# Kernel tuning notes

Hardware: AMD Instinct MI355X
Metric: run time of the kernel (lower is better)

## Reference

```python
import jax, jax.numpy as jnp
import numpy as np

B, S, D, E, K = 4, 4096, 2048, 64, 2


def setup_inputs() -> dict:
    key = jax.random.key(0)
    kx, kwg, kwn, kn = jax.random.split(key, 4)
    scale = 1.0 / np.sqrt(D)
    return {
        "x": jax.random.normal(kx, (B, S, D), dtype=jnp.float32),
        "Wg": jax.random.normal(kwg, (E, D), dtype=jnp.float32) * scale,
        "bg": jnp.zeros((E,), dtype=jnp.float32),
        "Wn": jax.random.normal(kwn, (E, D), dtype=jnp.float32) * scale,
        "bn": jnp.zeros((E,), dtype=jnp.float32),
        "noise": jax.random.normal(kn, (B, S, E), dtype=jnp.float32),
    }


def reference(x, Wg, bg, Wn, bn, noise):
    # gate / noise projections: [B,S,D] @ [D,E] -> [B,S,E]
    gate_logits = jnp.einsum("bsd,ed->bse", x, Wg) + bg
    noise_std = jax.nn.softplus(jnp.einsum("bsd,ed->bse", x, Wn) + bn)
    noisy_logits = gate_logits + noise * noise_std  # training-mode path

    # top-k over experts, then scatter back with -inf elsewhere
    flat = noisy_logits.reshape(-1, E)  # [T, E], T = B*S
    top_vals, top_idx = jax.lax.top_k(flat, K)  # [T, K]
    T = flat.shape[0]
    neg_inf = jnp.full((T, E), -jnp.inf, dtype=flat.dtype)
    full_logits = neg_inf.at[jnp.arange(T)[:, None], top_idx].set(top_vals)

    gate_probs = jax.nn.softmax(full_logits, axis=-1).reshape(B, S, E)
    top_k_indices = top_idx.reshape(B, S, K)
    return gate_probs, top_k_indices
```

## Files before the change

### kernel.cpp

```cpp
#include <hip/hip_runtime.h>
#include <math.h>
#include <stdint.h>

#define D_ 2048
#define E_ 64
#define T_ 16384

#define BM 32
#define BK 64
#define NT 32
#define ABUF_B 8192
#define BBUF_B 32768
#define BUF_B (ABUF_B + BBUF_B)
#define CT_STRIDE 132

typedef _Float16 h8 __attribute__((ext_vector_type(8)));
typedef float f16v __attribute__((ext_vector_type(16)));

__device__ __forceinline__ void split2(const float4& a, const float4& b,
                                       h8& h, h8& m) {
    const float xe[8] = {a.x, a.y, a.z, a.w, b.x, b.y, b.z, b.w};
#pragma unroll
    for (int i = 0; i < 8; ++i) {
        const _Float16 hh_ = (_Float16)xe[i];
        const float r = (xe[i] - (float)hh_) * 1024.0f;
        h[i] = hh_;
        m[i] = (_Float16)r;
    }
}

__device__ __forceinline__ void gload16(const void* g, void* l) {
    __builtin_amdgcn_global_load_lds(
        (const __attribute__((address_space(1))) uint32_t*)g,
        (__attribute__((address_space(3))) uint32_t*)l, 16, 0, 0);
}

__device__ __forceinline__ void topk_epilogue(float g, float nl, float nz,
                                              int lane, size_t tg,
                                              float* __restrict__ out_probs,
                                              float* __restrict__ out_idx) {
    const float sp = fmaxf(nl, 0.f) + log1pf(expf(-fabsf(nl)));
    const float noisy = g + nz * sp;

    float v = noisy;
    int idx = lane;
#pragma unroll
    for (int off = 32; off > 0; off >>= 1) {
        const float ov = __shfl_xor(v, off);
        const int oi = __shfl_xor(idx, off);
        if (ov > v || (ov == v && oi < idx)) { v = ov; idx = oi; }
    }
    const float v1 = v;
    const int i1 = idx;
    v = (lane == i1) ? -INFINITY : noisy;
    idx = lane;
#pragma unroll
    for (int off = 32; off > 0; off >>= 1) {
        const float ov = __shfl_xor(v, off);
        const int oi = __shfl_xor(idx, off);
        if (ov > v || (ov == v && oi < idx)) { v = ov; idx = oi; }
    }
    const float v2 = v;
    const int i2 = idx;

    const float e2 = expf(v2 - v1);
    const float denom = 1.f + e2;
    const float p = (lane == i1) ? (1.f / denom)
                                 : ((lane == i2) ? (e2 / denom) : 0.f);
    out_probs[tg * E_ + lane] = p;
    if (lane == 0) {
        out_idx[tg * 2 + 0] = (float)i1;
        out_idx[tg * 2 + 1] = (float)i2;
    }
}

__global__ void w_split_kernel(const float* __restrict__ Wg,
                               const float* __restrict__ Wn,
                               h8* __restrict__ wsp) {
    const int idx = blockIdx.x * blockDim.x + threadIdx.x;
    const int lane = idx & 63;
    const int s = (idx >> 6) & 127;
    const int f = idx >> 13;
    const int n = f * 32 + (lane & 31);
    const int k0 = s * 16 + ((lane >> 5) << 3);
    const float* src = (n < 64) ? &Wg[(size_t)n * D_ + k0]
                                : &Wn[(size_t)(n - 64) * D_ + k0];
    h8 hv, mv;
#pragma unroll
    for (int i = 0; i < 8; ++i) {
        const float w = src[i];
        const _Float16 wh = (_Float16)w;
        const float r = (w - (float)wh) * 1024.0f;
        hv[i] = wh;
        mv[i] = (_Float16)r;
    }
    wsp[0 * 32768 + idx] = hv;
    wsp[1 * 32768 + idx] = mv;
}

__launch_bounds__(512)
__global__ void gemm_topk_kernel(const float* __restrict__ x,
                                 const h8* __restrict__ wsp,
                                 const float* __restrict__ bg,
                                 const float* __restrict__ bn,
                                 const float* __restrict__ noise,
                                 float* __restrict__ out_probs,
                                 float* __restrict__ out_idx) {
    __shared__ __align__(16) char smem[2 * BUF_B];
    const int tid = threadIdx.x;
    const int lane = tid & 63;
    const int wv = tid >> 6;
    const int kh = wv >> 2;
    const int wn = wv & 3;
    const int block_m0 = blockIdx.x * BM;
    const char* wb = (const char*)wsp;

    const int ks_s = tid >> 6;
    const int sl = tid & 63;
    const float* asrc = x + (size_t)(block_m0 + (sl & 31)) * D_
                          + (ks_s & 3) * 16 + ((sl >> 5) << 3);
    const int aw_hi = (0 * 4 + (ks_s & 3)) * 1024 + sl * 16;
    const int aw_mid = (1 * 4 + (ks_s & 3)) * 1024 + sl * 16;

    f16v hh = {}, cx = {};

    auto STAGE_B = [&](int t, int b) {
        char* Bb = smem + b * BUF_B + ABUF_B;
#pragma unroll
        for (int j = 0; j < 4; ++j) {
            const int rid = wv * 4 + j;
            const int p = rid >> 4, f = (rid & 15) >> 2, ks = rid & 3;
            gload16(wb + ((size_t)(p * 32768 + f * 8192 + (t * 4 + ks) * 64 + lane)) * 16,
                    Bb + rid * 1024 + lane * 16);
        }
    };
    auto ALOAD = [&](int t, float4& ra, float4& rb) {
        if (tid < 256) {
            ra = *(const float4*)(asrc + t * BK);
            rb = *(const float4*)(asrc + t * BK + 4);
        }
    };
    auto ASPLIT = [&](const float4& ra, const float4& rb, int b) {
        if (tid < 256) {
            h8 hv, mv;
            split2(ra, rb, hv, mv);
            char* Ab = smem + b * BUF_B;
            *(h8*)(Ab + aw_hi) = hv;
            *(h8*)(Ab + aw_mid) = mv;
        }
    };
    auto COMPUTE = [&](int b) {
        const char* Ab = smem + b * BUF_B;
        const char* Bb = Ab + ABUF_B;
#pragma unroll
        for (int ksl = 0; ksl < 2; ++ksl) {
            const int ks = kh * 2 + ksl;
            const h8 ah = *(const h8*)(Ab + (0 * 4 + ks) * 1024 + lane * 16);
            const h8 am = *(const h8*)(Ab + (1 * 4 + ks) * 1024 + lane * 16);
            const h8 bh = *(const h8*)(Bb + ((0 * 16 + wn * 4 + ks)) * 1024 + lane * 16);
            const h8 bm = *(const h8*)(Bb + ((1 * 16 + wn * 4 + ks)) * 1024 + lane * 16);
            hh = __builtin_amdgcn_mfma_f32_32x32x16_f16(ah, bh, hh, 0, 0, 0);
            cx = __builtin_amdgcn_mfma_f32_32x32x16_f16(ah, bm, cx, 0, 0, 0);
            cx = __builtin_amdgcn_mfma_f32_32x32x16_f16(am, bh, cx, 0, 0, 0);
        }
    };

    float4 ra0{}, rb0{}, ra1{}, rb1{};
    ALOAD(0, ra0, rb0);
    STAGE_B(0, 0);
    ASPLIT(ra0, rb0, 0);
    ALOAD(1, ra0, rb0);
    __syncthreads();

#pragma unroll 1
    for (int i = 0; i < NT / 2; ++i) {
        const int t = 2 * i;
        STAGE_B(t + 1, 1);
        if (t + 2 < NT) ALOAD(t + 2, ra1, rb1);
        COMPUTE(0);
        ASPLIT(ra0, rb0, 1);
        __syncthreads();
        if (t + 2 < NT) STAGE_B(t + 2, 0);
        if (t + 3 < NT) ALOAD(t + 3, ra0, rb0);
        COMPUTE(1);
        if (t + 2 < NT) ASPLIT(ra1, rb1, 0);
        __syncthreads();
    }

    float* Ct = (float*)smem;
    {
        const float S1 = 1.0f / 1024.0f;
        const int col = wn * 32 + (lane & 31);
        const int rbase = 4 * (lane >> 5);
        if (kh == 0) {
#pragma unroll
            for (int r = 0; r < 16; ++r) {
                const int row = (r & 3) + 8 * (r >> 2) + rbase;
                Ct[row * CT_STRIDE + col] = hh[r] + cx[r] * S1;
            }
        }
        __syncthreads();
        if (kh == 1) {
#pragma unroll
            for (int r = 0; r < 16; ++r) {
                const int row = (r & 3) + 8 * (r >> 2) + rbase;
                Ct[row * CT_STRIDE + col] += hh[r] + cx[r] * S1;
            }
        }
        __syncthreads();
    }

    const float my_bg = bg[lane];
    const float my_bn = bn[lane];
#pragma unroll 1
    for (int tt = 0; tt < 4; ++tt) {
        const int tl = wv * 4 + tt;
        const size_t tg = (size_t)block_m0 + tl;
        const float g = Ct[tl * CT_STRIDE + lane] + my_bg;
        const float nl = Ct[tl * CT_STRIDE + 64 + lane] + my_bn;
        const float nz = noise[tg * E_ + lane];
        topk_epilogue(g, nl, nz, lane, tg, out_probs, out_idx);
    }
}

#define FBM 64
#define FBK 32
#define XS_STRIDE 68
#define WS_STRIDE 132
#define FCT_STRIDE 132

__launch_bounds__(256)
__global__ void noisy_topk_f32_kernel(const float* __restrict__ x,
                                      const float* __restrict__ Wg,
                                      const float* __restrict__ bg,
                                      const float* __restrict__ Wn,
                                      const float* __restrict__ bn,
                                      const float* __restrict__ noise,
                                      float* __restrict__ out_probs,
                                      float* __restrict__ out_idx) {
    __shared__ float smem[FBM * FCT_STRIDE];
    float* Xs = smem;
    float* Ws = smem + FBK * XS_STRIDE;

    const int tid = threadIdx.x;
    const int block_m0 = blockIdx.x * FBM;
    const int n0 = (tid & 31) * 4;
    const int m0 = (tid >> 5) * 8;

    float acc[8][4];
#pragma unroll
    for (int i = 0; i < 8; ++i)
#pragma unroll
        for (int j = 0; j < 4; ++j) acc[i][j] = 0.f;

    const int sj = tid & 7;
    const int sr = tid >> 3;

    for (int k0 = 0; k0 < D_; k0 += FBK) {
        __syncthreads();
#pragma unroll
        for (int it = 0; it < 2; ++it) {
            const int m = sr + it * 32;
            const float4 v = *reinterpret_cast<const float4*>(
                &x[(size_t)(block_m0 + m) * D_ + k0 + 4 * sj]);
            Xs[(4 * sj + 0) * XS_STRIDE + m] = v.x;
            Xs[(4 * sj + 1) * XS_STRIDE + m] = v.y;
            Xs[(4 * sj + 2) * XS_STRIDE + m] = v.z;
            Xs[(4 * sj + 3) * XS_STRIDE + m] = v.w;
        }
#pragma unroll
        for (int it = 0; it < 4; ++it) {
            const int n = sr + it * 32;
            const float* wrow = (n < 64) ? &Wg[(size_t)n * D_] : &Wn[(size_t)(n - 64) * D_];
            const float4 v = *reinterpret_cast<const float4*>(&wrow[k0 + 4 * sj]);
            Ws[(4 * sj + 0) * WS_STRIDE + n] = v.x;
            Ws[(4 * sj + 1) * WS_STRIDE + n] = v.y;
            Ws[(4 * sj + 2) * WS_STRIDE + n] = v.z;
            Ws[(4 * sj + 3) * WS_STRIDE + n] = v.w;
        }
        __syncthreads();
#pragma unroll
        for (int k = 0; k < FBK; ++k) {
            const float4 a0 = *reinterpret_cast<const float4*>(&Xs[k * XS_STRIDE + m0]);
            const float4 a1 = *reinterpret_cast<const float4*>(&Xs[k * XS_STRIDE + m0 + 4]);
            const float4 b4 = *reinterpret_cast<const float4*>(&Ws[k * WS_STRIDE + n0]);
            const float am[8] = {a0.x, a0.y, a0.z, a0.w, a1.x, a1.y, a1.z, a1.w};
            const float bb[4] = {b4.x, b4.y, b4.z, b4.w};
#pragma unroll
            for (int i = 0; i < 8; ++i)
#pragma unroll
                for (int j = 0; j < 4; ++j)
                    acc[i][j] = fmaf(am[i], bb[j], acc[i][j]);
        }
    }

    __syncthreads();
    float* Ct = smem;
#pragma unroll
    for (int i = 0; i < 8; ++i)
#pragma unroll
        for (int j = 0; j < 4; ++j)
            Ct[(m0 + i) * FCT_STRIDE + n0 + j] = acc[i][j];
    __syncthreads();

    const int wave = tid >> 6;
    const int lane = tid & 63;
    const float my_bg = bg[lane];
    const float my_bn = bn[lane];
#pragma unroll 1
    for (int tt = 0; tt < 16; ++tt) {
        const int tl = wave * 16 + tt;
        const size_t tg = (size_t)block_m0 + tl;
        const float g = Ct[tl * FCT_STRIDE + lane] + my_bg;
        const float nl = Ct[tl * FCT_STRIDE + 64 + lane] + my_bn;
        const float nz = noise[tg * E_ + lane];
        topk_epilogue(g, nl, nz, lane, tg, out_probs, out_idx);
    }
}

extern "C" void kernel_launch(void* const* d_in, const int* in_sizes, int n_in,
                              void* d_out, int out_size, void* d_ws, size_t ws_size,
                              hipStream_t stream) {
    const float* x = (const float*)d_in[0];
    const float* Wg = (const float*)d_in[1];
    const float* bg = (const float*)d_in[2];
    const float* Wn = (const float*)d_in[3];
    const float* bn = (const float*)d_in[4];
    const float* noise = (const float*)d_in[5];
    float* out_probs = (float*)d_out;
    float* out_idx = out_probs + (size_t)T_ * E_;

    const size_t WSP_BYTES = (size_t)2 * 32768 * 16;
    if (ws_size >= WSP_BYTES) {
        h8* wsp = (h8*)d_ws;
        hipLaunchKernelGGL(w_split_kernel, dim3(128), dim3(256), 0, stream, Wg, Wn, wsp);
        hipLaunchKernelGGL(gemm_topk_kernel, dim3(T_ / BM), dim3(512), 0, stream,
                           x, wsp, bg, bn, noise, out_probs, out_idx);
    } else {
        hipLaunchKernelGGL(noisy_topk_f32_kernel, dim3(T_ / FBM), dim3(256), 0, stream,
                           x, Wg, bg, Wn, bn, noise, out_probs, out_idx);
    }
}
```

Baseline: 61.12 us.

## Double M tile to 64 rows, split waves over M instead of K

```diff
diff --git a/kernel.cpp b/kernel.cpp
--- a/kernel.cpp
+++ b/kernel.cpp
@@ -6,10 +6,10 @@
 #define E_ 64
 #define T_ 16384
 
-#define BM 32
+#define BM 64
 #define BK 64
 #define NT 32
-#define ABUF_B 8192
+#define ABUF_B 16384
 #define BBUF_B 32768
 #define BUF_B (ABUF_B + BBUF_B)
 #define CT_STRIDE 132
@@ -33,6 +33,15 @@
     __builtin_amdgcn_global_load_lds(
         (const __attribute__((address_space(1))) uint32_t*)g,
         (__attribute__((address_space(3))) uint32_t*)l, 16, 0, 0);
+}
+
+__device__ __forceinline__ float4 nt_load4(const float* p) {
+    float4 r;
+    r.x = __builtin_nontemporal_load(p + 0);
+    r.y = __builtin_nontemporal_load(p + 1);
+    r.z = __builtin_nontemporal_load(p + 2);
+    r.w = __builtin_nontemporal_load(p + 3);
+    return r;
 }
 
 __device__ __forceinline__ void topk_epilogue(float g, float nl, float nz,
@@ -110,17 +119,19 @@
     const int tid = threadIdx.x;
     const int lane = tid & 63;
     const int wv = tid >> 6;
-    const int kh = wv >> 2;
+    const int mh = wv >> 2;
     const int wn = wv & 3;
     const int block_m0 = blockIdx.x * BM;
     const char* wb = (const char*)wsp;
 
-    const int ks_s = tid >> 6;
+    const int smf = tid >> 8;
+    const int sks = (tid >> 6) & 3;
     const int sl = tid & 63;
-    const float* asrc = x + (size_t)(block_m0 + (sl & 31)) * D_
-                          + (ks_s & 3) * 16 + ((sl >> 5) << 3);
-    const int aw_hi = (0 * 4 + (ks_s & 3)) * 1024 + sl * 16;
-    const int aw_mid = (1 * 4 + (ks_s & 3)) * 1024 + sl * 16;
+    const int srow = smf * 32 + (sl & 31);
+    const float* asrc = x + (size_t)(block_m0 + srow) * D_
+                          + sks * 16 + ((sl >> 5) << 3);
+    const int aw_hi = (0 * 8 + smf * 4 + sks) * 1024 + sl * 16;
+    const int aw_mid = (1 * 8 + smf * 4 + sks) * 1024 + sl * 16;
 
     f16v hh = {}, cx = {};
 
@@ -135,37 +146,32 @@
         }
     };
     auto ALOAD = [&](int t, float4& ra, float4& rb) {
-        if (tid < 256) {
-            ra = *(const float4*)(asrc + t * BK);
-            rb = *(const float4*)(asrc + t * BK + 4);
-        }
+        ra = nt_load4(asrc + t * BK);
+        rb = nt_load4(asrc + t * BK + 4);
     };
     auto ASPLIT = [&](const float4& ra, const float4& rb, int b) {
-        if (tid < 256) {
-            h8 hv, mv;
-            split2(ra, rb, hv, mv);
-            char* Ab = smem + b * BUF_B;
-            *(h8*)(Ab + aw_hi) = hv;
-            *(h8*)(Ab + aw_mid) = mv;
-        }
+        h8 hv, mv;
+        split2(ra, rb, hv, mv);
+        char* Ab = smem + b * BUF_B;
+        *(h8*)(Ab + aw_hi) = hv;
+        *(h8*)(Ab + aw_mid) = mv;
     };
     auto COMPUTE = [&](int b) {
         const char* Ab = smem + b * BUF_B;
         const char* Bb = Ab + ABUF_B;
 #pragma unroll
-        for (int ksl = 0; ksl < 2; ++ksl) {
-            const int ks = kh * 2 + ksl;
-            const h8 ah = *(const h8*)(Ab + (0 * 4 + ks) * 1024 + lane * 16);
-            const h8 am = *(const h8*)(Ab + (1 * 4 + ks) * 1024 + lane * 16);
-            const h8 bh = *(const h8*)(Bb + ((0 * 16 + wn * 4 + ks)) * 1024 + lane * 16);
-            const h8 bm = *(const h8*)(Bb + ((1 * 16 + wn * 4 + ks)) * 1024 + lane * 16);
+        for (int ks = 0; ks < 4; ++ks) {
+            const h8 ah = *(const h8*)(Ab + (0 * 8 + mh * 4 + ks) * 1024 + lane * 16);
+            const h8 am = *(const h8*)(Ab + (1 * 8 + mh * 4 + ks) * 1024 + lane * 16);
+            const h8 bh = *(const h8*)(Bb + (0 * 16 + wn * 4 + ks) * 1024 + lane * 16);
+            const h8 bm = *(const h8*)(Bb + (1 * 16 + wn * 4 + ks) * 1024 + lane * 16);
             hh = __builtin_amdgcn_mfma_f32_32x32x16_f16(ah, bh, hh, 0, 0, 0);
             cx = __builtin_amdgcn_mfma_f32_32x32x16_f16(ah, bm, cx, 0, 0, 0);
             cx = __builtin_amdgcn_mfma_f32_32x32x16_f16(am, bh, cx, 0, 0, 0);
         }
     };
 
-    float4 ra0{}, rb0{}, ra1{}, rb1{};
+    float4 ra0, rb0, ra1, rb1;
     ALOAD(0, ra0, rb0);
     STAGE_B(0, 0);
     ASPLIT(ra0, rb0, 0);
@@ -192,29 +198,19 @@
         const float S1 = 1.0f / 1024.0f;
         const int col = wn * 32 + (lane & 31);
         const int rbase = 4 * (lane >> 5);
-        if (kh == 0) {
-#pragma unroll
-            for (int r = 0; r < 16; ++r) {
-                const int row = (r & 3) + 8 * (r >> 2) + rbase;
-                Ct[row * CT_STRIDE + col] = hh[r] + cx[r] * S1;
-            }
-        }
-        __syncthreads();
-        if (kh == 1) {
-#pragma unroll
-            for (int r = 0; r < 16; ++r) {
-                const int row = (r & 3) + 8 * (r >> 2) + rbase;
-                Ct[row * CT_STRIDE + col] += hh[r] + cx[r] * S1;
-            }
-        }
-        __syncthreads();
-    }
+#pragma unroll
+        for (int r = 0; r < 16; ++r) {
+            const int row = mh * 32 + (r & 3) + 8 * (r >> 2) + rbase;
+            Ct[row * CT_STRIDE + col] = hh[r] + cx[r] * S1;
+        }
+    }
+    __syncthreads();
 
     const float my_bg = bg[lane];
     const float my_bn = bn[lane];
 #pragma unroll 1
-    for (int tt = 0; tt < 4; ++tt) {
-        const int tl = wv * 4 + tt;
+    for (int tt = 0; tt < 8; ++tt) {
+        const int tl = wv * 8 + tt;
         const size_t tg = (size_t)block_m0 + tl;
         const float g = Ct[tl * CT_STRIDE + lane] + my_bg;
         const float nl = Ct[tl * CT_STRIDE + 64 + lane] + my_bn;
```

Measured after the change: 84.11 us. 1.38x slower.
